# Kernel tuning notes

Hardware: AMD Instinct MI355X
Metric: run time of the kernel (lower is better)

Reference implementation:

```python
import jax, jax.numpy as jnp
import numpy as np

N_SENT = 131072
NUM_BAGS = 8192
REL_DIM = 690
NUM_CLASSES = 53


def setup_inputs() -> dict:
    key = jax.random.key(0)
    k1, k2, k3, k4, k5, k6 = jax.random.split(key, 6)
    x = jax.random.normal(k1, (N_SENT, REL_DIM), dtype=jnp.float32)
    relation_weight = jax.random.normal(k2, (NUM_CLASSES, REL_DIM), dtype=jnp.float32) * 0.06
    attention_weight = jax.random.normal(k3, (NUM_CLASSES, REL_DIM), dtype=jnp.float32) * 0.06
    bias = jax.random.normal(k4, (NUM_CLASSES,), dtype=jnp.float32)
    attention_query = jax.random.randint(k5, (N_SENT,), 0, NUM_CLASSES, dtype=jnp.int32)
    # strictly increasing bag boundaries: 0 < b_1 < ... < b_{B-1} < N
    interior = jax.random.choice(k6, N_SENT - 1, shape=(NUM_BAGS - 1,), replace=False) + 1
    scope = jnp.concatenate([jnp.zeros((1,), jnp.int32),
                             jnp.sort(interior).astype(jnp.int32),
                             jnp.full((1,), N_SENT, jnp.int32)])
    return {"x": x, "relation_weight": relation_weight,
            "attention_weight": attention_weight, "bias": bias,
            "attention_query": attention_query, "scope": scope}


def reference(x, relation_weight, attention_weight, bias, attention_query, scope):
    N = x.shape[0]
    B = scope.shape[0] - 1  # num bags
    # map each sentence to its bag: scope[b] <= i < scope[b+1]
    seg = jnp.searchsorted(scope[1:], jnp.arange(N), side="right")

    # per-sentence attention logit: sum(x * att_emb * rel_emb) over feature dim
    rel_q = relation_weight[attention_query]   # [N, D]
    att_q = attention_weight[attention_query]  # [N, D]
    logit = jnp.sum(x * att_q * rel_q, axis=1)  # [N]

    # segment softmax over each bag (numerically stable)
    seg_max = jax.ops.segment_max(logit, seg, num_segments=B)  # [B]
    e = jnp.exp(logit - seg_max[seg])                           # [N]
    denom = jax.ops.segment_sum(e, seg, num_segments=B)        # [B]
    w = e / denom[seg]                                          # [N]

    # attention-weighted bag representation
    bag_repre = jax.ops.segment_sum(w[:, None] * x, seg, num_segments=B)  # [B, D]

    # dropout with drop_prob = 0.0 -> identity
    logits = bag_repre @ relation_weight.T + bias  # [B, C]
    return logits
```

## Files before the change

kernel.cpp:

```cpp
#include <hip/hip_runtime.h>
#include <math.h>

#define NSENT 131072
#define NBAGS 8192
#define DIM   690
#define NCLS  53
#define PAIRS 345

__global__ void comb_kernel(const float* __restrict__ att,
                            const float* __restrict__ rel,
                            float* __restrict__ comb) {
    int i = blockIdx.x * 256 + threadIdx.x;
    if (i < NCLS * DIM) comb[i] = att[i] * rel[i];
}

template <bool USE_COMB>
__global__ __launch_bounds__(256, 8) void bag_attn_wave_kernel(
        const float* __restrict__ x,
        const float* __restrict__ rel,
        const float* __restrict__ att,
        const float* __restrict__ bias,
        const int*   __restrict__ query,
        const int*   __restrict__ scope,
        const float* __restrict__ comb,
        float*       __restrict__ out) {
    const int tid  = threadIdx.x;
    const int wave = tid >> 6;
    const int lane = tid & 63;
    const int b    = blockIdx.x * 4 + wave;

    const int start = scope[b];
    const int end   = scope[b + 1];

    float2 acc[6];
#pragma unroll
    for (int k = 0; k < 6; ++k) acc[k] = make_float2(0.f, 0.f);
    float m = -INFINITY;
    float l = 0.f;

    for (int i = start; i < end; ++i) {
        const float2* xrow = (const float2*)(x + (size_t)i * DIM);
        const int q = query[i];

        float2 xv[6];
        float partial = 0.f;
        if (USE_COMB) {
            const float2* crow = (const float2*)(comb + (size_t)q * DIM);
#pragma unroll
            for (int k = 0; k < 6; ++k) {
                const int p = lane + 64 * k;
                if (p < PAIRS) {
                    xv[k] = xrow[p];
                    const float2 cv = crow[p];
                    partial = fmaf(xv[k].x, cv.x, partial);
                    partial = fmaf(xv[k].y, cv.y, partial);
                } else {
                    xv[k] = make_float2(0.f, 0.f);
                }
            }
        } else {
            const float2* rrow = (const float2*)(rel + (size_t)q * DIM);
            const float2* arow = (const float2*)(att + (size_t)q * DIM);
#pragma unroll
            for (int k = 0; k < 6; ++k) {
                const int p = lane + 64 * k;
                if (p < PAIRS) {
                    xv[k] = xrow[p];
                    const float2 rv = rrow[p];
                    const float2 av = arow[p];
                    partial = fmaf(xv[k].x, rv.x * av.x, partial);
                    partial = fmaf(xv[k].y, rv.y * av.y, partial);
                } else {
                    xv[k] = make_float2(0.f, 0.f);
                }
            }
        }

#pragma unroll
        for (int off = 32; off >= 1; off >>= 1)
            partial += __shfl_xor(partial, off, 64);

        const float d = partial - m;
        if (d <= 8.0f) {
            const float e = __expf(d);
#pragma unroll
            for (int k = 0; k < 6; ++k) {
                acc[k].x = fmaf(e, xv[k].x, acc[k].x);
                acc[k].y = fmaf(e, xv[k].y, acc[k].y);
            }
            l += e;
        } else {
            const float r = __expf(-d);
#pragma unroll
            for (int k = 0; k < 6; ++k) {
                acc[k].x = fmaf(acc[k].x, r, xv[k].x);
                acc[k].y = fmaf(acc[k].y, r, xv[k].y);
            }
            l = fmaf(l, r, 1.f);
            m = partial;
        }
    }

    const float inv = 1.f / l;
    float res = (lane < NCLS) ? bias[lane] : 0.f;

#pragma unroll 1
    for (int c = 0; c < NCLS - 1; c += 2) {
        const float2* r0 = (const float2*)(rel + (size_t)c * DIM);
        const float2* r1 = (const float2*)(rel + (size_t)(c + 1) * DIM);
        float p0 = 0.f, p1 = 0.f;
#pragma unroll
        for (int k = 0; k < 6; ++k) {
            const int p = lane + 64 * k;
            if (p < PAIRS) {
                const float2 v0 = r0[p];
                const float2 v1 = r1[p];
                p0 = fmaf(v0.x, acc[k].x, p0);
                p0 = fmaf(v0.y, acc[k].y, p0);
                p1 = fmaf(v1.x, acc[k].x, p1);
                p1 = fmaf(v1.y, acc[k].y, p1);
            }
        }
#pragma unroll
        for (int off = 32; off >= 1; off >>= 1) {
            p0 += __shfl_xor(p0, off, 64);
            p1 += __shfl_xor(p1, off, 64);
        }
        if (lane == c)     res = fmaf(p0, inv, res);
        if (lane == c + 1) res = fmaf(p1, inv, res);
    }
    {
        const int c = NCLS - 1;
        const float2* r0 = (const float2*)(rel + (size_t)c * DIM);
        float p0 = 0.f;
#pragma unroll
        for (int k = 0; k < 6; ++k) {
            const int p = lane + 64 * k;
            if (p < PAIRS) {
                const float2 v0 = r0[p];
                p0 = fmaf(v0.x, acc[k].x, p0);
                p0 = fmaf(v0.y, acc[k].y, p0);
            }
        }
#pragma unroll
        for (int off = 32; off >= 1; off >>= 1)
            p0 += __shfl_xor(p0, off, 64);
        if (lane == c) res = fmaf(p0, inv, res);
    }

    if (lane < NCLS) out[(size_t)b * NCLS + lane] = res;
}

extern "C" void kernel_launch(void* const* d_in, const int* in_sizes, int n_in,
                              void* d_out, int out_size, void* d_ws, size_t ws_size,
                              hipStream_t stream) {
    const float* x     = (const float*)d_in[0];
    const float* rel   = (const float*)d_in[1];
    const float* att   = (const float*)d_in[2];
    const float* bias  = (const float*)d_in[3];
    const int*   query = (const int*)d_in[4];
    const int*   scope = (const int*)d_in[5];
    float*       out   = (float*)d_out;

    const size_t comb_bytes = (size_t)NCLS * DIM * sizeof(float);
    if (ws_size >= comb_bytes) {
        float* comb = (float*)d_ws;
        comb_kernel<<<(NCLS * DIM + 255) / 256, 256, 0, stream>>>(att, rel, comb);
        bag_attn_wave_kernel<true><<<NBAGS / 4, 256, 0, stream>>>(
            x, rel, att, bias, query, scope, comb, out);
    } else {
        bag_attn_wave_kernel<false><<<NBAGS / 4, 256, 0, stream>>>(
            x, rel, att, bias, query, scope, nullptr, out);
    }
}
```

Baseline: 685.1 us.

## Split bag attention into separate logits pass and per-bag softmax-weighted sum

Computes per-sentence attention logits in a dedicated kernel and writes them to workspace, then a per-bag kernel does max/sum reductions over stored logits and a dependency-free weighted accumulation of x before projecting to classes. This removes the serial per-row dot-product reduction and online-softmax rescaling from the bag loop, exposing more memory-level parallelism. It costs a second full read of x and extra workspace, and falls back to the fused kernel when workspace is small.

```diff
diff --git a/kernel.cpp b/kernel.cpp
--- a/kernel.cpp
+++ b/kernel.cpp
@@ -7,11 +7,150 @@
 #define NCLS  53
 #define PAIRS 345
 
+#define COMB_BYTES  (NCLS * DIM * 4)
+#define LOGITS_OFF  153600
+#define WS_NEEDED   (LOGITS_OFF + NSENT * 4)
+
 __global__ void comb_kernel(const float* __restrict__ att,
                             const float* __restrict__ rel,
                             float* __restrict__ comb) {
     int i = blockIdx.x * 256 + threadIdx.x;
     if (i < NCLS * DIM) comb[i] = att[i] * rel[i];
+}
+
+__global__ __launch_bounds__(256, 8) void logits_kernel(
+        const float* __restrict__ x,
+        const float* __restrict__ comb,
+        const int*   __restrict__ query,
+        float*       __restrict__ logits) {
+    const int lane = threadIdx.x & 63;
+    const int wid  = (blockIdx.x * 256 + threadIdx.x) >> 6;
+    const int i0   = wid * 16;
+
+#pragma unroll 1
+    for (int i = i0; i < i0 + 16; i += 2) {
+        const int q0 = query[i];
+        const int q1 = query[i + 1];
+        const float2* x0 = (const float2*)(x + (size_t)i * DIM);
+        const float2* x1 = (const float2*)(x + (size_t)(i + 1) * DIM);
+        const float2* c0 = (const float2*)(comb + (size_t)q0 * DIM);
+        const float2* c1 = (const float2*)(comb + (size_t)q1 * DIM);
+
+        float p0 = 0.f, p1 = 0.f;
+#pragma unroll
+        for (int k = 0; k < 6; ++k) {
+            const int p = lane + 64 * k;
+            if (p < PAIRS) {
+                const float2 a0 = x0[p], b0 = c0[p];
+                const float2 a1 = x1[p], b1 = c1[p];
+                p0 = fmaf(a0.x, b0.x, fmaf(a0.y, b0.y, p0));
+                p1 = fmaf(a1.x, b1.x, fmaf(a1.y, b1.y, p1));
+            }
+        }
+#pragma unroll
+        for (int off = 32; off >= 1; off >>= 1) {
+            p0 += __shfl_xor(p0, off, 64);
+            p1 += __shfl_xor(p1, off, 64);
+        }
+        if (lane == 0) {
+            logits[i]     = p0;
+            logits[i + 1] = p1;
+        }
+    }
+}
+
+__global__ __launch_bounds__(64, 4) void bag_kernel(
+        const float* __restrict__ x,
+        const float* __restrict__ rel,
+        const float* __restrict__ bias,
+        const float* __restrict__ logits,
+        const int*   __restrict__ scope,
+        float*       __restrict__ out) {
+    const int b    = blockIdx.x;
+    const int lane = threadIdx.x;
+    const int start = scope[b];
+    const int end   = scope[b + 1];
+
+    float mymax = -INFINITY;
+    for (int i = start + lane; i < end; i += 64) mymax = fmaxf(mymax, logits[i]);
+#pragma unroll
+    for (int off = 32; off >= 1; off >>= 1)
+        mymax = fmaxf(mymax, __shfl_xor(mymax, off, 64));
+
+    float mysum = 0.f;
+    for (int i = start + lane; i < end; i += 64)
+        mysum += __expf(logits[i] - mymax);
+#pragma unroll
+    for (int off = 32; off >= 1; off >>= 1)
+        mysum += __shfl_xor(mysum, off, 64);
+    const float invL = 1.f / mysum;
+
+    float2 acc[6];
+#pragma unroll
+    for (int k = 0; k < 6; ++k) acc[k] = make_float2(0.f, 0.f);
+
+#pragma unroll 2
+    for (int i = start; i < end; ++i) {
+        const float w = __expf(logits[i] - mymax) * invL;
+        const float2* xrow = (const float2*)(x + (size_t)i * DIM);
+#pragma unroll
+        for (int k = 0; k < 6; ++k) {
+            const int p = lane + 64 * k;
+            if (p < PAIRS) {
+                const float2 xv = xrow[p];
+                acc[k].x = fmaf(w, xv.x, acc[k].x);
+                acc[k].y = fmaf(w, xv.y, acc[k].y);
+            }
+        }
+    }
+
+    float res = (lane < NCLS) ? bias[lane] : 0.f;
+
+#pragma unroll 1
+    for (int c = 0; c < NCLS - 1; c += 2) {
+        const float2* r0 = (const float2*)(rel + (size_t)c * DIM);
+        const float2* r1 = (const float2*)(rel + (size_t)(c + 1) * DIM);
+        float p0 = 0.f, p1 = 0.f;
+#pragma unroll
+        for (int k = 0; k < 6; ++k) {
+            const int p = lane + 64 * k;
+            if (p < PAIRS) {
+                const float2 v0 = r0[p];
+                const float2 v1 = r1[p];
+                p0 = fmaf(v0.x, acc[k].x, p0);
+                p0 = fmaf(v0.y, acc[k].y, p0);
+                p1 = fmaf(v1.x, acc[k].x, p1);
+                p1 = fmaf(v1.y, acc[k].y, p1);
+            }
+        }
+#pragma unroll
+        for (int off = 32; off >= 1; off >>= 1) {
+            p0 += __shfl_xor(p0, off, 64);
+            p1 += __shfl_xor(p1, off, 64);
+        }
+        if (lane == c)     res += p0;
+        if (lane == c + 1) res += p1;
+    }
+    {
+        const int c = NCLS - 1;
+        const float2* r0 = (const float2*)(rel + (size_t)c * DIM);
+        float p0 = 0.f;
+#pragma unroll
+        for (int k = 0; k < 6; ++k) {
+            const int p = lane + 64 * k;
+            if (p < PAIRS) {
+                const float2 v0 = r0[p];
+                p0 = fmaf(v0.x, acc[k].x, p0);
+                p0 = fmaf(v0.y, acc[k].y, p0);
+            }
+        }
+#pragma unroll
+        for (int off = 32; off >= 1; off >>= 1)
+            p0 += __shfl_xor(p0, off, 64);
+        if (lane == c) res += p0;
+    }
+
+    if (lane < NCLS) out[(size_t)b * NCLS + lane] = res;
 }
 
 template <bool USE_COMB>
@@ -54,9 +193,7 @@
                     const float2 cv = crow[p];
                     partial = fmaf(xv[k].x, cv.x, partial);
                     partial = fmaf(xv[k].y, cv.y, partial);
-                } else {
-                    xv[k] = make_float2(0.f, 0.f);
-                }
+                } else xv[k] = make_float2(0.f, 0.f);
             }
         } else {
             const float2* rrow = (const float2*)(rel + (size_t)q * DIM);
@@ -70,12 +207,9 @@
                     const float2 av = arow[p];
                     partial = fmaf(xv[k].x, rv.x * av.x, partial);
                     partial = fmaf(xv[k].y, rv.y * av.y, partial);
-                } else {
-                    xv[k] = make_float2(0.f, 0.f);
-                }
-            }
-        }
-
+                } else xv[k] = make_float2(0.f, 0.f);
+            }
+        }
 #pragma unroll
         for (int off = 32; off >= 1; off >>= 1)
             partial += __shfl_xor(partial, off, 64);
@@ -103,7 +237,6 @@
 
     const float inv = 1.f / l;
     float res = (lane < NCLS) ? bias[lane] : 0.f;
-
 #pragma unroll 1
     for (int c = 0; c < NCLS - 1; c += 2) {
         const float2* r0 = (const float2*)(rel + (size_t)c * DIM);
@@ -147,7 +280,6 @@
             p0 += __shfl_xor(p0, off, 64);
         if (lane == c) res = fmaf(p0, inv, res);
     }
-
     if (lane < NCLS) out[(size_t)b * NCLS + lane] = res;
 }
 
@@ -162,8 +294,13 @@
     const int*   scope = (const int*)d_in[5];
     float*       out   = (float*)d_out;
 
-    const size_t comb_bytes = (size_t)NCLS * DIM * sizeof(float);
-    if (ws_size >= comb_bytes) {
+    if (ws_size >= (size_t)WS_NEEDED) {
+        float* comb   = (float*)d_ws;
+        float* logits = (float*)((char*)d_ws + LOGITS_OFF);
+        comb_kernel<<<(NCLS * DIM + 255) / 256, 256, 0, stream>>>(att, rel, comb);
+        logits_kernel<<<NSENT / (16 * 4), 256, 0, stream>>>(x, comb, query, logits);
+        bag_kernel<<<NBAGS, 64, 0, stream>>>(x, rel, bias, logits, scope, out);
+    } else if (ws_size >= (size_t)COMB_BYTES) {
         float* comb = (float*)d_ws;
         comb_kernel<<<(NCLS * DIM + 255) / 256, 256, 0, stream>>>(att, rel, comb);
         bag_attn_wave_kernel<true><<<NBAGS / 4, 256, 0, stream>>>(
```

Measured after the change: 884.8 us. +29.1%, slower.

## Split bag attention into two-pass chunked logits then weighted accumulation

Applied to the files above, without the earlier changes.

Replaces the per-row online softmax with a chunked two-pass scheme. Each wave first computes logits for up to 512 rows, two rows at a time for more memory parallelism, and stores them in shared memory. It then computes the chunk max and the exp weights, and re-reads x to accumulate the weighted sum. This removes the serial dependency of each row on the reduction result before accumulating, but reads each x row twice (the second read may hit cache) and lowers the launch-bounds occupancy hint from 8 to 4.

```diff
diff --git a/kernel.cpp b/kernel.cpp
--- a/kernel.cpp
+++ b/kernel.cpp
@@ -6,6 +6,9 @@
 #define DIM   690
 #define NCLS  53
 #define PAIRS 345
+#define MAXS  512
+
+#define COMB_BYTES  (NCLS * DIM * 4)
 
 __global__ void comb_kernel(const float* __restrict__ att,
                             const float* __restrict__ rel,
@@ -15,7 +18,7 @@
 }
 
 template <bool USE_COMB>
-__global__ __launch_bounds__(256, 8) void bag_attn_wave_kernel(
+__global__ __launch_bounds__(256, 4) void bag_fused_kernel(
         const float* __restrict__ x,
         const float* __restrict__ rel,
         const float* __restrict__ att,
@@ -29,6 +32,9 @@
     const int lane = tid & 63;
     const int b    = blockIdx.x * 4 + wave;
 
+    __shared__ float s_lgt[4][MAXS];
+    float* lgt = s_lgt[wave];
+
     const int start = scope[b];
     const int end   = scope[b + 1];
 
@@ -38,66 +44,128 @@
     float m = -INFINITY;
     float l = 0.f;
 
-    for (int i = start; i < end; ++i) {
-        const float2* xrow = (const float2*)(x + (size_t)i * DIM);
-        const int q = query[i];
-
-        float2 xv[6];
-        float partial = 0.f;
-        if (USE_COMB) {
-            const float2* crow = (const float2*)(comb + (size_t)q * DIM);
+    for (int cs = start; cs < end; cs += MAXS) {
+        const int ce = (end < cs + MAXS) ? end : (cs + MAXS);
+        const int n  = ce - cs;
+
+        int i = cs;
+        for (; i + 1 < ce; i += 2) {
+            const int q0 = query[i];
+            const int q1 = query[i + 1];
+            const float2* x0 = (const float2*)(x + (size_t)i * DIM);
+            const float2* x1 = (const float2*)(x + (size_t)(i + 1) * DIM);
+            float p0 = 0.f, p1 = 0.f;
+            if (USE_COMB) {
+                const float2* c0 = (const float2*)(comb + (size_t)q0 * DIM);
+                const float2* c1 = (const float2*)(comb + (size_t)q1 * DIM);
+#pragma unroll
+                for (int k = 0; k < 6; ++k) {
+                    const int p = lane + 64 * k;
+                    if (p < PAIRS) {
+                        const float2 a0 = x0[p], b0 = c0[p];
+                        const float2 a1 = x1[p], b1 = c1[p];
+                        p0 = fmaf(a0.x, b0.x, fmaf(a0.y, b0.y, p0));
+                        p1 = fmaf(a1.x, b1.x, fmaf(a1.y, b1.y, p1));
+                    }
+                }
+            } else {
+                const float2* r0 = (const float2*)(rel + (size_t)q0 * DIM);
+                const float2* a0r = (const float2*)(att + (size_t)q0 * DIM);
+                const float2* r1 = (const float2*)(rel + (size_t)q1 * DIM);
+                const float2* a1r = (const float2*)(att + (size_t)q1 * DIM);
+#pragma unroll
+                for (int k = 0; k < 6; ++k) {
+                    const int p = lane + 64 * k;
+                    if (p < PAIRS) {
+                        const float2 a0 = x0[p], rv0 = r0[p], av0 = a0r[p];
+                        const float2 a1 = x1[p], rv1 = r1[p], av1 = a1r[p];
+                        p0 = fmaf(a0.x, rv0.x * av0.x, fmaf(a0.y, rv0.y * av0.y, p0));
+                        p1 = fmaf(a1.x, rv1.x * av1.x, fmaf(a1.y, rv1.y * av1.y, p1));
+                    }
+                }
+            }
+#pragma unroll
+            for (int off = 32; off >= 1; off >>= 1) {
+                p0 += __shfl_xor(p0, off, 64);
+                p1 += __shfl_xor(p1, off, 64);
+            }
+            if (lane == 0) {
+                lgt[i - cs]     = p0;
+                lgt[i - cs + 1] = p1;
+            }
+        }
+        if (i < ce) {
+            const int q0 = query[i];
+            const float2* x0 = (const float2*)(x + (size_t)i * DIM);
+            float p0 = 0.f;
+            if (USE_COMB) {
+                const float2* c0 = (const float2*)(comb + (size_t)q0 * DIM);
+#pragma unroll
+                for (int k = 0; k < 6; ++k) {
+                    const int p = lane + 64 * k;
+                    if (p < PAIRS) {
+                        const float2 a0 = x0[p], b0 = c0[p];
+                        p0 = fmaf(a0.x, b0.x, fmaf(a0.y, b0.y, p0));
+                    }
+                }
+            } else {
+                const float2* r0 = (const float2*)(rel + (size_t)q0 * DIM);
+                const float2* a0r = (const float2*)(att + (size_t)q0 * DIM);
+#pragma unroll
+                for (int k = 0; k < 6; ++k) {
+                    const int p = lane + 64 * k;
+                    if (p < PAIRS) {
+                        const float2 a0 = x0[p], rv0 = r0[p], av0 = a0r[p];
+                        p0 = fmaf(a0.x, rv0.x * av0.x, fmaf(a0.y, rv0.y * av0.y, p0));
+                    }
+                }
+            }
+#pragma unroll
+            for (int off = 32; off >= 1; off >>= 1)
+                p0 += __shfl_xor(p0, off, 64);
+            if (lane == 0) lgt[i - cs] = p0;
+        }
+
+        float cm = -INFINITY;
+        for (int j = lane; j < n; j += 64) cm = fmaxf(cm, lgt[j]);
+#pragma unroll
+        for (int off = 32; off >= 1; off >>= 1)
+            cm = fmaxf(cm, __shfl_xor(cm, off, 64));
+
+        const float Mn = fmaxf(m, cm);
+        const float r  = __expf(m - Mn);
+        l *= r;
+#pragma unroll
+        for (int k = 0; k < 6; ++k) {
+            acc[k].x *= r;
+            acc[k].y *= r;
+        }
+        m = Mn;
+
+        float ps = 0.f;
+        for (int j = lane; j < n; j += 64) {
+            const float w = __expf(lgt[j] - Mn);
+            lgt[j] = w;
+            ps += w;
+        }
+#pragma unroll
+        for (int off = 32; off >= 1; off >>= 1)
+            ps += __shfl_xor(ps, off, 64);
+        l += ps;
+
+#pragma unroll 2
+        for (int i2 = cs; i2 < ce; ++i2) {
+            const float w = lgt[i2 - cs];
+            const float2* xr = (const float2*)(x + (size_t)i2 * DIM);
 #pragma unroll
             for (int k = 0; k < 6; ++k) {
                 const int p = lane + 64 * k;
                 if (p < PAIRS) {
-                    xv[k] = xrow[p];
-                    const float2 cv = crow[p];
-                    partial = fmaf(xv[k].x, cv.x, partial);
-                    partial = fmaf(xv[k].y, cv.y, partial);
-                } else {
-                    xv[k] = make_float2(0.f, 0.f);
-                }
-            }
-        } else {
-            const float2* rrow = (const float2*)(rel + (size_t)q * DIM);
-            const float2* arow = (const float2*)(att + (size_t)q * DIM);
-#pragma unroll
-            for (int k = 0; k < 6; ++k) {
-                const int p = lane + 64 * k;
-                if (p < PAIRS) {
-                    xv[k] = xrow[p];
-                    const float2 rv = rrow[p];
-                    const float2 av = arow[p];
-                    partial = fmaf(xv[k].x, rv.x * av.x, partial);
-                    partial = fmaf(xv[k].y, rv.y * av.y, partial);
-                } else {
-                    xv[k] = make_float2(0.f, 0.f);
-                }
-            }
-        }
-
-#pragma unroll
-        for (int off = 32; off >= 1; off >>= 1)
-            partial += __shfl_xor(partial, off, 64);
-
-        const float d = partial - m;
-        if (d <= 8.0f) {
-            const float e = __expf(d);
-#pragma unroll
-            for (int k = 0; k < 6; ++k) {
-                acc[k].x = fmaf(e, xv[k].x, acc[k].x);
-                acc[k].y = fmaf(e, xv[k].y, acc[k].y);
-            }
-            l += e;
-        } else {
-            const float r = __expf(-d);
-#pragma unroll
-            for (int k = 0; k < 6; ++k) {
-                acc[k].x = fmaf(acc[k].x, r, xv[k].x);
-                acc[k].y = fmaf(acc[k].y, r, xv[k].y);
-            }
-            l = fmaf(l, r, 1.f);
-            m = partial;
+                    const float2 xv = xr[p];
+                    acc[k].x = fmaf(w, xv.x, acc[k].x);
+                    acc[k].y = fmaf(w, xv.y, acc[k].y);
+                }
+            }
         }
     }
 
@@ -162,14 +230,13 @@
     const int*   scope = (const int*)d_in[5];
     float*       out   = (float*)d_out;
 
-    const size_t comb_bytes = (size_t)NCLS * DIM * sizeof(float);
-    if (ws_size >= comb_bytes) {
+    if (ws_size >= (size_t)COMB_BYTES) {
         float* comb = (float*)d_ws;
         comb_kernel<<<(NCLS * DIM + 255) / 256, 256, 0, stream>>>(att, rel, comb);
-        bag_attn_wave_kernel<true><<<NBAGS / 4, 256, 0, stream>>>(
+        bag_fused_kernel<true><<<NBAGS / 4, 256, 0, stream>>>(
             x, rel, att, bias, query, scope, comb, out);
     } else {
-        bag_attn_wave_kernel<false><<<NBAGS / 4, 256, 0, stream>>>(
+        bag_fused_kernel<false><<<NBAGS / 4, 256, 0, stream>>>(
             x, rel, att, bias, query, scope, nullptr, out);
     }
 }
```

Measured after the change: 687.7 us. Within noise of the previous version (+0.4%).

## Split each bag across four waves with shared-memory softmax merge

Applied to the files above, without the earlier changes.

Each bag now gets a whole 256-thread block instead of one wave. Each wave handles two sentences per step, strided by eight, and keeps its own online-softmax state. The four partial states are merged through shared memory, and the final class projection is split across the waves. This shortens the serial per-bag chain and adds memory-level parallelism, which should help load imbalance from large bags. The cost is extra block synchronisation, shared-memory use, and four times as many blocks.

```diff
diff --git a/kernel.cpp b/kernel.cpp
--- a/kernel.cpp
+++ b/kernel.cpp
@@ -6,6 +6,8 @@
 #define DIM   690
 #define NCLS  53
 #define PAIRS 345
+
+#define COMB_BYTES  (NCLS * DIM * 4)
 
 __global__ void comb_kernel(const float* __restrict__ att,
                             const float* __restrict__ rel,
@@ -15,7 +17,7 @@
 }
 
 template <bool USE_COMB>
-__global__ __launch_bounds__(256, 8) void bag_attn_wave_kernel(
+__global__ __launch_bounds__(256, 5) void bag_attn4_kernel(
         const float* __restrict__ x,
         const float* __restrict__ rel,
         const float* __restrict__ att,
@@ -27,7 +29,7 @@
     const int tid  = threadIdx.x;
     const int wave = tid >> 6;
     const int lane = tid & 63;
-    const int b    = blockIdx.x * 4 + wave;
+    const int b    = blockIdx.x;
 
     const int start = scope[b];
     const int end   = scope[b + 1];
@@ -38,76 +40,156 @@
     float m = -INFINITY;
     float l = 0.f;
 
-    for (int i = start; i < end; ++i) {
-        const float2* xrow = (const float2*)(x + (size_t)i * DIM);
-        const int q = query[i];
-
-        float2 xv[6];
-        float partial = 0.f;
+    for (int i = start + 2 * wave; i < end; i += 8) {
+        const bool two = (i + 1 < end);
+        const int  i1  = two ? i + 1 : i;
+        const int  q0  = query[i];
+        const int  q1  = query[i1];
+        const float2* xr0 = (const float2*)(x + (size_t)i  * DIM);
+        const float2* xr1 = (const float2*)(x + (size_t)i1 * DIM);
+
+        float2 xv0[6], xv1[6];
+        float p0 = 0.f, p1 = 0.f;
         if (USE_COMB) {
-            const float2* crow = (const float2*)(comb + (size_t)q * DIM);
+            const float2* c0 = (const float2*)(comb + (size_t)q0 * DIM);
+            const float2* c1 = (const float2*)(comb + (size_t)q1 * DIM);
 #pragma unroll
             for (int k = 0; k < 6; ++k) {
                 const int p = lane + 64 * k;
                 if (p < PAIRS) {
-                    xv[k] = xrow[p];
-                    const float2 cv = crow[p];
-                    partial = fmaf(xv[k].x, cv.x, partial);
-                    partial = fmaf(xv[k].y, cv.y, partial);
+                    xv0[k] = xr0[p];
+                    xv1[k] = xr1[p];
+                    const float2 cv0 = c0[p];
+                    const float2 cv1 = c1[p];
+                    p0 = fmaf(xv0[k].x, cv0.x, fmaf(xv0[k].y, cv0.y, p0));
+                    p1 = fmaf(xv1[k].x, cv1.x, fmaf(xv1[k].y, cv1.y, p1));
                 } else {
-                    xv[k] = make_float2(0.f, 0.f);
+                    xv0[k] = make_float2(0.f, 0.f);
+                    xv1[k] = make_float2(0.f, 0.f);
                 }
             }
         } else {
-            const float2* rrow = (const float2*)(rel + (size_t)q * DIM);
-            const float2* arow = (const float2*)(att + (size_t)q * DIM);
+            const float2* r0 = (const float2*)(rel + (size_t)q0 * DIM);
+            const float2* a0 = (const float2*)(att + (size_t)q0 * DIM);
+            const float2* r1 = (const float2*)(rel + (size_t)q1 * DIM);
+            const float2* a1 = (const float2*)(att + (size_t)q1 * DIM);
 #pragma unroll
             for (int k = 0; k < 6; ++k) {
                 const int p = lane + 64 * k;
                 if (p < PAIRS) {
-                    xv[k] = xrow[p];
-                    const float2 rv = rrow[p];
-                    const float2 av = arow[p];
-                    partial = fmaf(xv[k].x, rv.x * av.x, partial);
-                    partial = fmaf(xv[k].y, rv.y * av.y, partial);
+                    xv0[k] = xr0[p];
+                    xv1[k] = xr1[p];
+                    const float2 rv0 = r0[p], av0 = a0[p];
+                    const float2 rv1 = r1[p], av1 = a1[p];
+                    p0 = fmaf(xv0[k].x, rv0.x * av0.x, fmaf(xv0[k].y, rv0.y * av0.y, p0));
+                    p1 = fmaf(xv1[k].x, rv1.x * av1.x, fmaf(xv1[k].y, rv1.y * av1.y, p1));
                 } else {
-                    xv[k] = make_float2(0.f, 0.f);
-                }
-            }
-        }
-
-#pragma unroll
-        for (int off = 32; off >= 1; off >>= 1)
-            partial += __shfl_xor(partial, off, 64);
-
-        const float d = partial - m;
-        if (d <= 8.0f) {
-            const float e = __expf(d);
-#pragma unroll
-            for (int k = 0; k < 6; ++k) {
-                acc[k].x = fmaf(e, xv[k].x, acc[k].x);
-                acc[k].y = fmaf(e, xv[k].y, acc[k].y);
-            }
-            l += e;
+                    xv0[k] = make_float2(0.f, 0.f);
+                    xv1[k] = make_float2(0.f, 0.f);
+                }
+            }
+        }
+
+#pragma unroll
+        for (int off = 32; off >= 1; off >>= 1) {
+            p0 += __shfl_xor(p0, off, 64);
+            p1 += __shfl_xor(p1, off, 64);
+        }
+
+        if (two) {
+            const float d0 = p0 - m;
+            const float d1 = p1 - m;
+            if (d0 <= 8.0f && d1 <= 8.0f) {
+                const float e0 = __expf(d0);
+                const float e1 = __expf(d1);
+#pragma unroll
+                for (int k = 0; k < 6; ++k) {
+                    acc[k].x = fmaf(e0, xv0[k].x, fmaf(e1, xv1[k].x, acc[k].x));
+                    acc[k].y = fmaf(e0, xv0[k].y, fmaf(e1, xv1[k].y, acc[k].y));
+                }
+                l += e0 + e1;
+            } else {
+                const float mn = fmaxf(m, fmaxf(p0, p1));
+                const float r  = __expf(m - mn);
+                const float e0 = __expf(p0 - mn);
+                const float e1 = __expf(p1 - mn);
+#pragma unroll
+                for (int k = 0; k < 6; ++k) {
+                    acc[k].x = fmaf(acc[k].x, r, fmaf(e0, xv0[k].x, e1 * xv1[k].x));
+                    acc[k].y = fmaf(acc[k].y, r, fmaf(e0, xv0[k].y, e1 * xv1[k].y));
+                }
+                l = fmaf(l, r, e0 + e1);
+                m = mn;
+            }
         } else {
-            const float r = __expf(-d);
-#pragma unroll
-            for (int k = 0; k < 6; ++k) {
-                acc[k].x = fmaf(acc[k].x, r, xv[k].x);
-                acc[k].y = fmaf(acc[k].y, r, xv[k].y);
-            }
-            l = fmaf(l, r, 1.f);
-            m = partial;
-        }
-    }
-
-    const float inv = 1.f / l;
-    float res = (lane < NCLS) ? bias[lane] : 0.f;
+            const float d0 = p0 - m;
+            if (d0 <= 8.0f) {
+                const float e0 = __expf(d0);
+#pragma unroll
+                for (int k = 0; k < 6; ++k) {
+                    acc[k].x = fmaf(e0, xv0[k].x, acc[k].x);
+                    acc[k].y = fmaf(e0, xv0[k].y, acc[k].y);
+                }
+                l += e0;
+            } else {
+                const float mn = fmaxf(m, p0);
+                const float r  = __expf(m - mn);
+                const float e0 = __expf(p0 - mn);
+#pragma unroll
+                for (int k = 0; k < 6; ++k) {
+                    acc[k].x = fmaf(acc[k].x, r, e0 * xv0[k].x);
+                    acc[k].y = fmaf(acc[k].y, r, e0 * xv0[k].y);
+                }
+                l = fmaf(l, r, e0);
+                m = mn;
+            }
+        }
+    }
+
+    __shared__ float  s_m[4];
+    __shared__ float  s_l[4];
+    __shared__ float2 s_acc[4][PAIRS];
+
+    if (lane == 0) { s_m[wave] = m; s_l[wave] = l; }
+    __syncthreads();
+
+    const float M = fmaxf(fmaxf(s_m[0], s_m[1]), fmaxf(s_m[2], s_m[3]));
+    float Ltot = 0.f;
+#pragma unroll
+    for (int w = 0; w < 4; ++w) {
+        const float lw = s_l[w];
+        Ltot += (lw > 0.f) ? lw * __expf(s_m[w] - M) : 0.f;
+    }
+    const float factor = (l > 0.f) ? __expf(m - M) : 0.f;
+#pragma unroll
+    for (int k = 0; k < 6; ++k) {
+        const int p = lane + 64 * k;
+        if (p < PAIRS)
+            s_acc[wave][p] = make_float2(acc[k].x * factor, acc[k].y * factor);
+    }
+    __syncthreads();
+
+    const float inv = 1.f / Ltot;
+    float2 am[6];
+#pragma unroll
+    for (int k = 0; k < 6; ++k) {
+        const int p = lane + 64 * k;
+        if (p < PAIRS) {
+            const float2 a0 = s_acc[0][p], a1 = s_acc[1][p];
+            const float2 a2 = s_acc[2][p], a3 = s_acc[3][p];
+            am[k] = make_float2(((a0.x + a1.x) + (a2.x + a3.x)) * inv,
+                                ((a0.y + a1.y) + (a2.y + a3.y)) * inv);
+        } else {
+            am[k] = make_float2(0.f, 0.f);
+        }
+    }
 
 #pragma unroll 1
-    for (int c = 0; c < NCLS - 1; c += 2) {
-        const float2* r0 = (const float2*)(rel + (size_t)c * DIM);
-        const float2* r1 = (const float2*)(rel + (size_t)(c + 1) * DIM);
+    for (int c0 = wave; c0 < NCLS; c0 += 8) {
+        const int  c1 = c0 + 4;
+        const bool h2 = (c1 < NCLS);
+        const float2* r0 = (const float2*)(rel + (size_t)c0 * DIM);
+        const float2* r1 = (const float2*)(rel + (size_t)(h2 ? c1 : c0) * DIM);
         float p0 = 0.f, p1 = 0.f;
 #pragma unroll
         for (int k = 0; k < 6; ++k) {
@@ -115,10 +197,8 @@
             if (p < PAIRS) {
                 const float2 v0 = r0[p];
                 const float2 v1 = r1[p];
-                p0 = fmaf(v0.x, acc[k].x, p0);
-                p0 = fmaf(v0.y, acc[k].y, p0);
-                p1 = fmaf(v1.x, acc[k].x, p1);
-                p1 = fmaf(v1.y, acc[k].y, p1);
+                p0 = fmaf(v0.x, am[k].x, fmaf(v0.y, am[k].y, p0));
+                p1 = fmaf(v1.x, am[k].x, fmaf(v1.y, am[k].y, p1));
             }
         }
 #pragma unroll
@@ -126,29 +206,11 @@
             p0 += __shfl_xor(p0, off, 64);
             p1 += __shfl_xor(p1, off, 64);
         }
-        if (lane == c)     res = fmaf(p0, inv, res);
-        if (lane == c + 1) res = fmaf(p1, inv, res);
-    }
-    {
-        const int c = NCLS - 1;
-        const float2* r0 = (const float2*)(rel + (size_t)c * DIM);
-        float p0 = 0.f;
-#pragma unroll
-        for (int k = 0; k < 6; ++k) {
-            const int p = lane + 64 * k;
-            if (p < PAIRS) {
-                const float2 v0 = r0[p];
-                p0 = fmaf(v0.x, acc[k].x, p0);
-                p0 = fmaf(v0.y, acc[k].y, p0);
-            }
-        }
-#pragma unroll
-        for (int off = 32; off >= 1; off >>= 1)
-            p0 += __shfl_xor(p0, off, 64);
-        if (lane == c) res = fmaf(p0, inv, res);
-    }
-
-    if (lane < NCLS) out[(size_t)b * NCLS + lane] = res;
+        if (lane == 0) {
+            out[(size_t)b * NCLS + c0] = p0 + bias[c0];
+            if (h2) out[(size_t)b * NCLS + c1] = p1 + bias[c1];
+        }
+    }
 }
 
 extern "C" void kernel_launch(void* const* d_in, const int* in_sizes, int n_in,
@@ -162,14 +224,13 @@
     const int*   scope = (const int*)d_in[5];
     float*       out   = (float*)d_out;
 
-    const size_t comb_bytes = (size_t)NCLS * DIM * sizeof(float);
-    if (ws_size >= comb_bytes) {
+    if (ws_size >= (size_t)COMB_BYTES) {
         float* comb = (float*)d_ws;
         comb_kernel<<<(NCLS * DIM + 255) / 256, 256, 0, stream>>>(att, rel, comb);
-        bag_attn_wave_kernel<true><<<NBAGS / 4, 256, 0, stream>>>(
+        bag_attn4_kernel<true><<<NBAGS, 256, 0, stream>>>(
             x, rel, att, bias, query, scope, comb, out);
     } else {
-        bag_attn_wave_kernel<false><<<NBAGS / 4, 256, 0, stream>>>(
+        bag_attn4_kernel<false><<<NBAGS, 256, 0, stream>>>(
             x, rel, att, bias, query, scope, nullptr, out);
     }
 }
```

Result: faster. 595.2 us (-13.1%).
